# Performance work log

Hardware: AMD Instinct MI355X
Metric: run time of the kernel (lower is better)

## Reference

```python
import jax, jax.numpy as jnp
import numpy as np

V = 50_000        # nodes
E = 1_600_000     # edges (avg degree ~32)
DH = 128          # node feature dim == hidden_dim
DR = 3            # coordinate dim
NB = 16           # RBF bases
D_MIN, D_MAX = 0.0, 4.5


def setup_inputs() -> dict:
    key = jax.random.key(0)
    k1, k2, k3, k4, k5, k6 = jax.random.split(key, 6)
    node_feats = jax.random.normal(k1, (V, DH), jnp.float32)
    coords = jax.random.normal(k2, (V, DR), jnp.float32)
    src = jax.random.randint(k3, (E,), 0, V, dtype=jnp.int32)
    dest = jax.random.randint(k4, (E,), 0, V, dtype=jnp.int32)
    W1 = jax.random.normal(k5, (NB, DH), jnp.float32) / np.sqrt(NB)
    W2 = jax.random.normal(k6, (DH, DH), jnp.float32) / np.sqrt(DH)
    return {"node_feats": node_feats, "coords": coords, "src": src,
            "dest": dest, "W1": W1, "W2": W2}


def _rbf(d):
    # Gaussian RBF expansion of pairwise distances: [E] -> [E, NB]
    mu = jnp.linspace(D_MIN, D_MAX, NB, dtype=d.dtype)
    width = (D_MAX - D_MIN) / (NB - 1)
    coeff = -0.5 / (width * width)
    return jnp.exp(coeff * jnp.square(d[:, None] - mu))


def reference(node_feats, coords, src, dest, W1, W2):
    diff = coords[src] - coords[dest]                      # [E, DR]
    d_ij = jnp.sqrt(jnp.sum(diff * diff, axis=-1))         # [E]
    m_ij = jax.nn.relu(_rbf(d_ij) @ W1)                    # [E, DH]
    m_ij = jax.nn.relu(m_ij @ W2)                          # [E, DH]
    msg = node_feats[src] * m_ij                           # gather-multiply
    return jax.ops.segment_sum(msg, dest, num_segments=node_feats.shape[0])
```

## Files before the change

kernel.cpp:

```cpp
#include <hip/hip_runtime.h>


#define DHID 128
#define NBASE 16

constexpr int TE = 128;
constexpr int THREADS = 1024;

using f16x8 = __fp16 __attribute__((ext_vector_type(8)));
using f32x4 = float __attribute__((ext_vector_type(4)));


__global__ void zero_kernel(float4* __restrict__ out4, int n4,
                            int* __restrict__ cursor, int V) {
    for (int i = blockIdx.x * blockDim.x + threadIdx.x; i < n4;
         i += gridDim.x * blockDim.x)
        out4[i] = make_float4(0.f, 0.f, 0.f, 0.f);
    for (int i = blockIdx.x * blockDim.x + threadIdx.x; i < V;
         i += gridDim.x * blockDim.x)
        cursor[i] = 0;
}

__global__ void hist_kernel(const int* __restrict__ dstI, int E,
                            int* __restrict__ cursor) {
    for (int i = blockIdx.x * blockDim.x + threadIdx.x; i < E;
         i += gridDim.x * blockDim.x)
        atomicAdd(&cursor[dstI[i]], 1);
}

constexpr int SCAN_BS = 256;

__global__ __launch_bounds__(SCAN_BS)
void scan_partial(const int* __restrict__ cursor, int V, int* __restrict__ sums) {
    const int i = blockIdx.x * SCAN_BS + threadIdx.x;
    int v = (i < V) ? cursor[i] : 0;
#pragma unroll
    for (int off = 32; off; off >>= 1) v += __shfl_down(v, off, 64);
    __shared__ int ws[4];
    if ((threadIdx.x & 63) == 0) ws[threadIdx.x >> 6] = v;
    __syncthreads();
    if (threadIdx.x == 0) sums[blockIdx.x] = ws[0] + ws[1] + ws[2] + ws[3];
}

__global__ __launch_bounds__(SCAN_BS)
void scan_sums(int* __restrict__ sums, int nch) {
    const int tid = threadIdx.x;
    const int lane = tid & 63, w = tid >> 6;
    const int v = (tid < nch) ? sums[tid] : 0;
    int s = v;
#pragma unroll
    for (int off = 1; off < 64; off <<= 1) {
        const int n = __shfl_up(s, off, 64);
        if (lane >= off) s += n;
    }
    __shared__ int wt[4];
    if (lane == 63) wt[w] = s;
    __syncthreads();
    int off = 0;
    for (int j = 0; j < w; ++j) off += wt[j];
    if (tid < nch) sums[tid] = off + s - v;
}

__global__ __launch_bounds__(SCAN_BS)
void scan_apply(int* __restrict__ cursor, int V, const int* __restrict__ sums) {
    const int i = blockIdx.x * SCAN_BS + threadIdx.x;
    const int lane = threadIdx.x & 63, w = threadIdx.x >> 6;
    const int v = (i < V) ? cursor[i] : 0;
    int s = v;
#pragma unroll
    for (int off = 1; off < 64; off <<= 1) {
        const int n = __shfl_up(s, off, 64);
        if (lane >= off) s += n;
    }
    __shared__ int wt[4];
    if (lane == 63) wt[w] = s;
    __syncthreads();
    int off = sums[blockIdx.x];
    for (int j = 0; j < w; ++j) off += wt[j];
    if (i < V) cursor[i] = off + s - v;
}

__global__ void scatter_kernel(const int* __restrict__ dstI, int E,
                               int* __restrict__ cursor, int* __restrict__ perm) {
    for (int i = blockIdx.x * blockDim.x + threadIdx.x; i < E;
         i += gridDim.x * blockDim.x) {
        const int pos = atomicAdd(&cursor[dstI[i]], 1);
        perm[pos] = i;
    }
}


__global__ __launch_bounds__(THREADS, 8)
void cfconv_mfma(const float* __restrict__ node_feats,
                 const float* __restrict__ coords,
                 const int* __restrict__ srcI,
                 const int* __restrict__ dstI,
                 const float* __restrict__ W1,
                 const float* __restrict__ W2,
                 const int* __restrict__ perm,
                 float* __restrict__ out,
                 int E, int ntiles)
{
    __shared__ __align__(16) unsigned short sM1h[TE * DHID];
    __shared__ __align__(16) unsigned short sW2t[DHID * DHID];
    __shared__ int sSrc[TE];
    __shared__ int sDst[TE];

    const int tid = threadIdx.x;
    const int lane = tid & 63;
    const int w = tid >> 6;

    {
        const int c = tid & 127;
        const int kq = (tid >> 7) * 16;
        f16x8 lo, hi;
#pragma unroll
        for (int i = 0; i < 8; ++i) {
            lo[i] = (__fp16)W2[(kq + i) * DHID + c];
            hi[i] = (__fp16)W2[(kq + 8 + i) * DHID + c];
        }
        char* base = (char*)sW2t + c * 256;
        const int sw = (c & 7) << 4;
        *(f16x8*)(base + ((kq * 2) ^ sw)) = lo;
        *(f16x8*)(base + ((kq * 2 + 16) ^ sw)) = hi;
    }

    const int e1 = tid & 127;
    const int kg = tid >> 7;
    const int er = (w >> 2) * 32;
    const int cb = (w & 3) * 32;
    const int l15 = lane & 15;
    const int lg = lane >> 4;

    constexpr float WIDTH = 4.5f / 15.0f;
    constexpr float COEFF = -0.5f / (WIDTH * WIDTH);

    for (int tile = blockIdx.x; tile < ntiles; tile += gridDim.x) {
        const int ebase = tile * TE;
        __syncthreads();

        {
            int ge = ebase + e1;
            if (ge >= E) ge = E - 1;
            const int pe = perm[ge];
            const int s = srcI[pe];
            const int dv = dstI[pe];
            if (kg == 0) { sSrc[e1] = s; sDst[e1] = dv; }
            const float dx = coords[s * 3 + 0] - coords[dv * 3 + 0];
            const float dy = coords[s * 3 + 1] - coords[dv * 3 + 1];
            const float dz = coords[s * 3 + 2] - coords[dv * 3 + 2];
            const float d = sqrtf(fmaf(dx, dx, fmaf(dy, dy, dz * dz)));
            float rbf[NBASE];
#pragma unroll
            for (int b = 0; b < NBASE; ++b) {
                const float t = d - WIDTH * (float)b;
                rbf[b] = __expf(COEFF * t * t);
            }
            f16x8 lo, hi;
#pragma unroll
            for (int kk = 0; kk < 16; ++kk) {
                const int k = __builtin_amdgcn_readfirstlane(kg * 16 + kk);
                float a = 0.f;
#pragma unroll
                for (int b = 0; b < NBASE; ++b)
                    a = fmaf(rbf[b], W1[b * DHID + k], a);
                const __fp16 hv = (__fp16)fmaxf(a, 0.f);
                if (kk < 8) lo[kk] = hv; else hi[kk - 8] = hv;
            }
            char* base = (char*)sM1h + e1 * 256;
            const int sw = (e1 & 7) << 4;
            *(f16x8*)(base + ((kg * 32) ^ sw)) = lo;
            *(f16x8*)(base + ((kg * 32 + 16) ^ sw)) = hi;
        }
        __syncthreads();

        f32x4 q00 = {0.f,0.f,0.f,0.f};
        f32x4 q01 = {0.f,0.f,0.f,0.f};
        f32x4 q10 = {0.f,0.f,0.f,0.f};
        f32x4 q11 = {0.f,0.f,0.f,0.f};
        {
            const int ra0 = er + l15, ra1 = er + 16 + l15;
            const int rb0 = cb + l15, rb1 = cb + 16 + l15;
            const char* pa0 = (const char*)sM1h + ra0 * 256;
            const char* pa1 = (const char*)sM1h + ra1 * 256;
            const char* pb0 = (const char*)sW2t + rb0 * 256;
            const char* pb1 = (const char*)sW2t + rb1 * 256;
            const int sa0 = (ra0 & 7) << 4, sa1 = (ra1 & 7) << 4;
            const int sb0 = (rb0 & 7) << 4, sb1 = (rb1 & 7) << 4;
#pragma unroll
            for (int kb = 0; kb < 4; ++kb) {
                const int kbyte = kb * 64 + lg * 16;
                const f16x8 a0 = *(const f16x8*)(pa0 + (kbyte ^ sa0));
                const f16x8 a1 = *(const f16x8*)(pa1 + (kbyte ^ sa1));
                const f16x8 b0 = *(const f16x8*)(pb0 + (kbyte ^ sb0));
                const f16x8 b1 = *(const f16x8*)(pb1 + (kbyte ^ sb1));
                q00 = __builtin_amdgcn_mfma_f32_16x16x32_f16(b0, a0, q00, 0, 0, 0);
                q01 = __builtin_amdgcn_mfma_f32_16x16x32_f16(b0, a1, q01, 0, 0, 0);
                q10 = __builtin_amdgcn_mfma_f32_16x16x32_f16(b1, a0, q10, 0, 0, 0);
                q11 = __builtin_amdgcn_mfma_f32_16x16x32_f16(b1, a1, q11, 0, 0, 0);
            }
        }

#pragma unroll
        for (int ti = 0; ti < 2; ++ti) {
            const int e = er + ti * 16 + l15;
            const int dv = sDst[e];
            const int s = sSrc[e];
            bool pr1, pr2, pr4, pr8;
            {
                int nd;
                nd = __shfl_up(dv, 1, 16); pr1 = (l15 >= 1) && (nd == dv);
                nd = __shfl_up(dv, 2, 16); pr2 = (l15 >= 2) && (nd == dv);
                nd = __shfl_up(dv, 4, 16); pr4 = (l15 >= 4) && (nd == dv);
                nd = __shfl_up(dv, 8, 16); pr8 = (l15 >= 8) && (nd == dv);
            }
            const int ndn = __shfl_down(dv, 1, 16);
            const bool tail = (l15 == 15) || (ndn != dv);
#pragma unroll
            for (int tj = 0; tj < 2; ++tj) {
                const f32x4 q = tj ? (ti ? q11 : q10) : (ti ? q01 : q00);
                const int c0 = cb + tj * 16 + lg * 4;
                const float4 nf = *(const float4*)&node_feats[(size_t)s * DHID + c0];
                float m0 = fmaxf(q[0], 0.f) * nf.x;
                float m1 = fmaxf(q[1], 0.f) * nf.y;
                float m2 = fmaxf(q[2], 0.f) * nf.z;
                float m3 = fmaxf(q[3], 0.f) * nf.w;
                float t0, t1, t2, t3;
                t0 = __shfl_up(m0, 1, 16); t1 = __shfl_up(m1, 1, 16);
                t2 = __shfl_up(m2, 1, 16); t3 = __shfl_up(m3, 1, 16);
                if (pr1) { m0 += t0; m1 += t1; m2 += t2; m3 += t3; }
                t0 = __shfl_up(m0, 2, 16); t1 = __shfl_up(m1, 2, 16);
                t2 = __shfl_up(m2, 2, 16); t3 = __shfl_up(m3, 2, 16);
                if (pr2) { m0 += t0; m1 += t1; m2 += t2; m3 += t3; }
                t0 = __shfl_up(m0, 4, 16); t1 = __shfl_up(m1, 4, 16);
                t2 = __shfl_up(m2, 4, 16); t3 = __shfl_up(m3, 4, 16);
                if (pr4) { m0 += t0; m1 += t1; m2 += t2; m3 += t3; }
                t0 = __shfl_up(m0, 8, 16); t1 = __shfl_up(m1, 8, 16);
                t2 = __shfl_up(m2, 8, 16); t3 = __shfl_up(m3, 8, 16);
                if (pr8) { m0 += t0; m1 += t1; m2 += t2; m3 += t3; }
                if (tail) {
                    float* op = &out[(size_t)dv * DHID + c0];
                    atomicAdd(op + 0, m0);
                    atomicAdd(op + 1, m1);
                    atomicAdd(op + 2, m2);
                    atomicAdd(op + 3, m3);
                }
            }
        }
    }
}

extern "C" void kernel_launch(void* const* d_in, const int* in_sizes, int n_in,
                              void* d_out, int out_size, void* d_ws, size_t ws_size,
                              hipStream_t stream) {
    const float* node_feats = (const float*)d_in[0];
    const float* coords     = (const float*)d_in[1];
    const int*   srcI       = (const int*)d_in[2];
    const int*   dstI       = (const int*)d_in[3];
    const float* W1         = (const float*)d_in[4];
    const float* W2         = (const float*)d_in[5];
    float* out = (float*)d_out;

    const int E = in_sizes[2];
    const int V = in_sizes[0] / DHID;

    int* cursor = (int*)d_ws;
    int* perm   = cursor + V;
    const int nch = (V + SCAN_BS - 1) / SCAN_BS;
    int* sums   = perm + E;

    const int n4 = out_size / 4;
    zero_kernel<<<1024, 256, 0, stream>>>((float4*)out, n4, cursor, V);
    hist_kernel<<<2048, 256, 0, stream>>>(dstI, E, cursor);
    scan_partial<<<nch, SCAN_BS, 0, stream>>>(cursor, V, sums);
    scan_sums<<<1, SCAN_BS, 0, stream>>>(sums, nch);
    scan_apply<<<nch, SCAN_BS, 0, stream>>>(cursor, V, sums);
    scatter_kernel<<<2048, 256, 0, stream>>>(dstI, E, cursor, perm);

    const int ntiles = (E + TE - 1) / TE;
    const int grid = ntiles < 512 ? ntiles : 512;
    cfconv_mfma<<<grid, THREADS, 0, stream>>>(node_feats, coords, srcI, dstI,
                                              W1, W2, perm, out, E, ntiles);
}
```

Baseline: 699.7 us.

## Compute RBF-W1 layer with MFMA, double-buffer indices, fuse scan kernels

Each thread now computes two RBF bases and writes them to shared memory as fp16. The first layer (RBF @ W1) then runs as one MFMA per 16-edge group, with W1 held in registers, replacing 256 scalar FMAs per thread. The src/dst index arrays are double-buffered, which lets the tile loop drop its leading barrier. The separate scan_sums kernel is merged into scan_apply, where every block redundantly scans the chunk sums, saving one launch. The cost is fp16 rounding of the RBF values and an extra barrier and shared-memory round trip per tile.

```diff
diff --git a/kernel.cpp b/kernel.cpp
--- a/kernel.cpp
+++ b/kernel.cpp
@@ -8,6 +8,7 @@
 constexpr int THREADS = 1024;
 
 using f16x8 = __fp16 __attribute__((ext_vector_type(8)));
+using f16x4 = __fp16 __attribute__((ext_vector_type(4)));
 using f32x4 = float __attribute__((ext_vector_type(4)));
 
 
@@ -43,41 +44,41 @@
 }
 
 __global__ __launch_bounds__(SCAN_BS)
-void scan_sums(int* __restrict__ sums, int nch) {
-    const int tid = threadIdx.x;
-    const int lane = tid & 63, w = tid >> 6;
-    const int v = (tid < nch) ? sums[tid] : 0;
-    int s = v;
+void scan_apply(int* __restrict__ cursor, int V,
+                const int* __restrict__ sums, int nch) {
+    __shared__ int sIncl[SCAN_BS];
+    __shared__ int wt[4];
+    const int tid = threadIdx.x, lane = tid & 63, w = tid >> 6;
+    {
+        const int v = (tid < nch) ? sums[tid] : 0;
+        int s = v;
+#pragma unroll
+        for (int off = 1; off < 64; off <<= 1) {
+            const int n = __shfl_up(s, off, 64);
+            if (lane >= off) s += n;
+        }
+        if (lane == 63) wt[w] = s;
+        __syncthreads();
+        int wo = 0;
+        for (int j = 0; j < w; ++j) wo += wt[j];
+        sIncl[tid] = wo + s;
+        __syncthreads();
+    }
+    const int base = blockIdx.x ? sIncl[blockIdx.x - 1] : 0;
+    __syncthreads();
+    const int i = blockIdx.x * SCAN_BS + tid;
+    const int val = (i < V) ? cursor[i] : 0;
+    int s = val;
 #pragma unroll
     for (int off = 1; off < 64; off <<= 1) {
         const int n = __shfl_up(s, off, 64);
         if (lane >= off) s += n;
     }
-    __shared__ int wt[4];
     if (lane == 63) wt[w] = s;
     __syncthreads();
-    int off = 0;
-    for (int j = 0; j < w; ++j) off += wt[j];
-    if (tid < nch) sums[tid] = off + s - v;
-}
-
-__global__ __launch_bounds__(SCAN_BS)
-void scan_apply(int* __restrict__ cursor, int V, const int* __restrict__ sums) {
-    const int i = blockIdx.x * SCAN_BS + threadIdx.x;
-    const int lane = threadIdx.x & 63, w = threadIdx.x >> 6;
-    const int v = (i < V) ? cursor[i] : 0;
-    int s = v;
-#pragma unroll
-    for (int off = 1; off < 64; off <<= 1) {
-        const int n = __shfl_up(s, off, 64);
-        if (lane >= off) s += n;
-    }
-    __shared__ int wt[4];
-    if (lane == 63) wt[w] = s;
-    __syncthreads();
-    int off = sums[blockIdx.x];
-    for (int j = 0; j < w; ++j) off += wt[j];
-    if (i < V) cursor[i] = off + s - v;
+    int wo = 0;
+    for (int j = 0; j < w; ++j) wo += wt[j];
+    if (i < V) cursor[i] = base + wo + s - val;
 }
 
 __global__ void scatter_kernel(const int* __restrict__ dstI, int E,
@@ -103,8 +104,9 @@
 {
     __shared__ __align__(16) unsigned short sM1h[TE * DHID];
     __shared__ __align__(16) unsigned short sW2t[DHID * DHID];
-    __shared__ int sSrc[TE];
-    __shared__ int sDst[TE];
+    __shared__ __align__(16) unsigned int sRbf[TE * 12];
+    __shared__ int sSrc[2][TE];
+    __shared__ int sDst[2][TE];
 
     const int tid = threadIdx.x;
     const int lane = tid & 63;
@@ -127,17 +129,29 @@
 
     const int e1 = tid & 127;
     const int kg = tid >> 7;
+    const int l15 = lane & 15;
+    const int lg = lane >> 4;
+    const int kt = w >> 1;
+    const int etb = (w & 1) * 4;
     const int er = (w >> 2) * 32;
     const int cb = (w & 3) * 32;
-    const int l15 = lane & 15;
-    const int lg = lane >> 4;
+
+    f16x8 w1f;
+    {
+        const int k = kt * 16 + l15;
+#pragma unroll
+        for (int j = 0; j < 8; ++j) {
+            const float v = W1[((lg & 1) * 8 + j) * DHID + k];
+            w1f[j] = (lg < 2) ? (__fp16)v : (__fp16)0.f;
+        }
+    }
 
     constexpr float WIDTH = 4.5f / 15.0f;
     constexpr float COEFF = -0.5f / (WIDTH * WIDTH);
 
+    int pbuf = 0;
     for (int tile = blockIdx.x; tile < ntiles; tile += gridDim.x) {
         const int ebase = tile * TE;
-        __syncthreads();
 
         {
             int ge = ebase + e1;
@@ -145,32 +159,34 @@
             const int pe = perm[ge];
             const int s = srcI[pe];
             const int dv = dstI[pe];
-            if (kg == 0) { sSrc[e1] = s; sDst[e1] = dv; }
+            if (kg == 0) { sSrc[pbuf][e1] = s; sDst[pbuf][e1] = dv; }
             const float dx = coords[s * 3 + 0] - coords[dv * 3 + 0];
             const float dy = coords[s * 3 + 1] - coords[dv * 3 + 1];
             const float dz = coords[s * 3 + 2] - coords[dv * 3 + 2];
             const float d = sqrtf(fmaf(dx, dx, fmaf(dy, dy, dz * dz)));
-            float rbf[NBASE];
-#pragma unroll
-            for (int b = 0; b < NBASE; ++b) {
-                const float t = d - WIDTH * (float)b;
-                rbf[b] = __expf(COEFF * t * t);
+            const float t0 = d - WIDTH * (float)(2 * kg);
+            const float t1 = d - WIDTH * (float)(2 * kg + 1);
+            union { __fp16 h[2]; unsigned int u; } pk;
+            pk.h[0] = (__fp16)__expf(COEFF * t0 * t0);
+            pk.h[1] = (__fp16)__expf(COEFF * t1 * t1);
+            sRbf[e1 * 12 + kg] = pk.u;
+        }
+        __syncthreads();
+
+        {
+#pragma unroll
+            for (int i = 0; i < 4; ++i) {
+                const int e = (etb + i) * 16 + l15;
+                const f16x8 bf =
+                    *(const f16x8*)((const char*)sRbf + e * 48 + (lg & 1) * 16);
+                f32x4 d4 = {0.f, 0.f, 0.f, 0.f};
+                d4 = __builtin_amdgcn_mfma_f32_16x16x32_f16(w1f, bf, d4, 0, 0, 0);
+                f16x4 hv;
+#pragma unroll
+                for (int r = 0; r < 4; ++r) hv[r] = (__fp16)fmaxf(d4[r], 0.f);
+                char* p = (char*)sM1h + e * 256 + ((kt * 32 + lg * 8) ^ ((e & 7) << 4));
+                *(f16x4*)p = hv;
             }
-            f16x8 lo, hi;
-#pragma unroll
-            for (int kk = 0; kk < 16; ++kk) {
-                const int k = __builtin_amdgcn_readfirstlane(kg * 16 + kk);
-                float a = 0.f;
-#pragma unroll
-                for (int b = 0; b < NBASE; ++b)
-                    a = fmaf(rbf[b], W1[b * DHID + k], a);
-                const __fp16 hv = (__fp16)fmaxf(a, 0.f);
-                if (kk < 8) lo[kk] = hv; else hi[kk - 8] = hv;
-            }
-            char* base = (char*)sM1h + e1 * 256;
-            const int sw = (e1 & 7) << 4;
-            *(f16x8*)(base + ((kg * 32) ^ sw)) = lo;
-            *(f16x8*)(base + ((kg * 32 + 16) ^ sw)) = hi;
         }
         __syncthreads();
 
@@ -204,8 +220,8 @@
 #pragma unroll
         for (int ti = 0; ti < 2; ++ti) {
             const int e = er + ti * 16 + l15;
-            const int dv = sDst[e];
-            const int s = sSrc[e];
+            const int dv = sDst[pbuf][e];
+            const int s = sSrc[pbuf][e];
             bool pr1, pr2, pr4, pr8;
             {
                 int nd;
@@ -247,6 +263,7 @@
                 }
             }
         }
+        pbuf ^= 1;
     }
 }
 
@@ -273,8 +290,7 @@
     zero_kernel<<<1024, 256, 0, stream>>>((float4*)out, n4, cursor, V);
     hist_kernel<<<2048, 256, 0, stream>>>(dstI, E, cursor);
     scan_partial<<<nch, SCAN_BS, 0, stream>>>(cursor, V, sums);
-    scan_sums<<<1, SCAN_BS, 0, stream>>>(sums, nch);
-    scan_apply<<<nch, SCAN_BS, 0, stream>>>(cursor, V, sums);
+    scan_apply<<<nch, SCAN_BS, 0, stream>>>(cursor, V, sums, nch);
     scatter_kernel<<<2048, 256, 0, stream>>>(dstI, E, cursor, perm);
 
     const int ntiles = (E + TE - 1) / TE;
```

Result: no change. 700.7 us (+0.1%).
